# Optimization experiments

Measured on AMD Instinct MI355X. Metric: run time of the kernel, lower is better.

## Reference

```python
import jax, jax.numpy as jnp
import numpy as np

C_IN, D_MODEL, TAO, M = 7, 512, 3, 5
KERNELS = D_MODEL // C_IN              # 73
LEFTOUT = D_MODEL - C_IN * KERNELS     # 1
B, L = 32, 4096


def setup_inputs() -> dict:
    key = jax.random.key(0)
    k1, k2, k3, k4, k5 = jax.random.split(key, 5)
    x = jax.random.normal(k1, (B, L, C_IN), dtype=jnp.float32)
    # kaiming_normal fan_in, leaky_relu (negative_slope=0.01): gain^2/fan_in
    fan_in = (M + 1) * 3
    std = float(np.sqrt(2.0 / (fan_in * (1.0 + 0.01 ** 2))))
    conv_w = jax.random.normal(k2, (KERNELS, M + 1, 3), dtype=jnp.float32) * std
    bound = float(1.0 / np.sqrt(fan_in))
    conv_b = jax.random.uniform(k3, (KERNELS,), jnp.float32, -bound, bound)
    leftout_w = jax.random.uniform(k4, (LEFTOUT, M + 1, 3), jnp.float32, -bound, bound)
    leftout_b = jax.random.uniform(k5, (LEFTOUT,), jnp.float32, -bound, bound)
    return {"x": x, "conv_w": conv_w, "conv_b": conv_b,
            "leftout_w": leftout_w, "leftout_b": leftout_b}


def _circ_conv1d(inp, w, b):
    # inp: [N, Cin, L]; w: [Cout, Cin, 3]; circular padding of 1 on each side
    xp = jnp.concatenate([inp[..., -1:], inp, inp[..., :1]], axis=-1)
    y = jax.lax.conv_general_dilated(xp, w, window_strides=(1,), padding='VALID',
                                     dimension_numbers=('NCH', 'OIH', 'NCH'))
    return y + b[None, :, None]


def reference(x, conv_w, conv_b, leftout_w, leftout_b):
    b, n, c = x.shape  # [B, L, C_IN]
    # delay-coordinate embedding: emb[b, t, c, i] = x[b, t - i*tao, c], zero for t < m*tao
    idx = jnp.arange(n)[:, None] - jnp.arange(M + 1)[None, :] * TAO   # [L, m+1]
    g = x[:, jnp.clip(idx, 0, n - 1), :]                              # [B, L, m+1, C]
    valid = (jnp.arange(n) >= M * TAO)[None, :, None, None]
    g = jnp.where(valid, g, jnp.zeros((), x.dtype))
    # chunk j (over channels) is [B, m+1, L]; all share the same conv -> batch over B*C
    chunks = jnp.transpose(g, (0, 3, 2, 1))                           # [B, C, m+1, L]
    flat = chunks.reshape(b * c, M + 1, n)
    y = _circ_conv1d(flat, conv_w, conv_b).reshape(b, c * KERNELS, n)  # [B, C*K, L]
    y_left = _circ_conv1d(chunks[:, -1], leftout_w, leftout_b)         # [B, LEFTOUT, L]
    out = jnp.concatenate([y, y_left], axis=1)                         # [B, D_MODEL, L]
    return jnp.transpose(out, (0, 2, 1))                               # [B, L, D_MODEL]
```

## Files before the change

kernel.cpp:

```cpp
#include <hip/hip_runtime.h>

#define C_IN     7
#define D_MODEL  512
#define TAO      3
#define M_TAPS   5
#define KERNELS  73
#define B_SZ     32
#define L_SZ     4096
#define TB       64
#define NTB      (L_SZ / TB)
#define ROWS     (TB + 17)
#define SHIFT    3
#define RPAD     88
#define CHUNK    8
#define NCH      (TB / CHUNK)

__global__ __launch_bounds__(512, 6) void trc_conv_kernel(
    const float* __restrict__ x,
    const float* __restrict__ conv_w,
    const float* __restrict__ conv_b,
    const float* __restrict__ leftout_w,
    const float* __restrict__ leftout_b,
    float* __restrict__ out)
{
    __shared__ float xs[C_IN][RPAD];
    __shared__ __align__(16) float buf[8][2][CHUNK][64];

    const int tid = threadIdx.x;
    const int wv  = tid >> 6;
    const int ln  = tid & 63;
    const int b   = blockIdx.x / NTB;
    const int tb  = blockIdx.x % NTB;
    const int t0  = tb * TB;

    const float* xb = x + (size_t)b * L_SZ * C_IN;
    for (int i = tid; i < ROWS * C_IN; i += 512) {
        int r = i / C_IN, c = i - r * C_IN;
        int g = t0 - 16 + r;
        if (g < 0)      g += L_SZ;
        if (g >= L_SZ)  g -= L_SZ;
        xs[c][r + SHIFT] = xb[(size_t)g * C_IN + c];
    }
    __syncthreads();

    const int d = tid;
    int ch;
    const float* wsrc;
    float bias;
    if (d < C_IN * KERNELS) {
        ch = d / KERNELS;
        int o = d - ch * KERNELS;
        wsrc = conv_w + o * 18;
        bias = conv_b[o];
    } else {
        ch = C_IN - 1;
        wsrc = leftout_w;
        bias = leftout_b[0];
    }
    const float* __restrict__ rowp = &xs[ch][SHIFT];

    float wreg[18];
    #pragma unroll
    for (int j = 0; j < 18; ++j) {
        int k = j % 3;
        int m = (15 + k - j) / 3;
        wreg[j] = wsrc[m * 3 + k];
    }

    const bool first = (tb == 0), last = (tb == NTB - 1);

    auto edge_eval = [&](int tl) -> float {
        float acc = bias;
        #pragma unroll
        for (int k = 0; k < 3; ++k) {
            int tt = t0 + tl + k - 1;
            if (tt < 0)      tt += L_SZ;
            if (tt >= L_SZ)  tt -= L_SZ;
            if (tt >= M_TAPS * TAO) {
                int lt = tl + 15 + k;
                #pragma unroll
                for (int m = 0; m < 6; ++m)
                    acc = fmaf(rowp[lt - 3 * m], wreg[15 + k - 3 * m], acc);
            }
        }
        return acc;
    };

    float* __restrict__ bufw = &buf[wv][0][0][0];
    const int lr = ln >> 4, lc = ln & 15;
    float4* base4 = (float4*)(out + ((size_t)b * L_SZ + t0) * D_MODEL + wv * 64);

    float win[25];
    #pragma unroll
    for (int q = 0; q < 17; ++q) win[q] = rowp[q];

    float4 r0, r1;

    for (int c = 0; c < NCH; ++c) {
        float* __restrict__ bc = bufw + (c & 1) * (CHUNK * 64);

        {
            float4 f0 = *(const float4*)&rowp[8 * c + 17];
            float4 f1 = *(const float4*)&rowp[8 * c + 21];
            win[17] = f0.x; win[18] = f0.y; win[19] = f0.z; win[20] = f0.w;
            win[21] = f1.x; win[22] = f1.y; win[23] = f1.z; win[24] = f1.w;
        }

        #pragma unroll
        for (int i = 0; i < CHUNK; ++i) {
            float acc = bias;
            #pragma unroll
            for (int j = 0; j < 18; ++j)
                acc = fmaf(win[i + j], wreg[j], acc);
            bc[i * 64 + ln] = acc;
        }
        #pragma unroll
        for (int q = 0; q < 17; ++q) win[q] = win[q + 8];

        if (first && c < 2) {
            for (int i = 0; i < CHUNK; ++i)
                bc[i * 64 + ln] = edge_eval(c * CHUNK + i);
        }
        if (last && c == NCH - 1) {
            bc[(CHUNK - 1) * 64 + ln] = edge_eval(TB - 1);
        }

        const float4* bv = (const float4*)bc;
        float4 n0 = bv[ln];
        float4 n1 = bv[ln + 64];
        __builtin_amdgcn_sched_barrier(0);

        if (c > 0) {
            base4[(size_t)((c - 1) * CHUNK + 0 + lr) * (D_MODEL / 4) + lc] = r0;
            base4[(size_t)((c - 1) * CHUNK + 4 + lr) * (D_MODEL / 4) + lc] = r1;
        }
        r0 = n0; r1 = n1;
    }
    base4[(size_t)((NCH - 1) * CHUNK + 0 + lr) * (D_MODEL / 4) + lc] = r0;
    base4[(size_t)((NCH - 1) * CHUNK + 4 + lr) * (D_MODEL / 4) + lc] = r1;
}

extern "C" void kernel_launch(void* const* d_in, const int* in_sizes, int n_in,
                              void* d_out, int out_size, void* d_ws, size_t ws_size,
                              hipStream_t stream) {
    const float* x          = (const float*)d_in[0];
    const float* conv_w     = (const float*)d_in[1];
    const float* conv_b     = (const float*)d_in[2];
    const float* leftout_w  = (const float*)d_in[3];
    const float* leftout_b  = (const float*)d_in[4];
    float* out = (float*)d_out;

    dim3 grid(B_SZ * NTB);
    trc_conv_kernel<<<grid, 512, 0, stream>>>(x, conv_w, conv_b,
                                              leftout_w, leftout_b, out);
}
```

Baseline: 49.69 us.

## Add dedicated store wavefront with block-wide double-buffered LDS staging

Adds a ninth wavefront that acts as a producer-consumer store engine. The 8 compute waves write each 8-row chunk into a shared block-wide double buffer, and the store wave writes full 2 KB output rows to global memory. Compute and store waves synchronize with a block barrier per chunk. This is meant to decouple global stores from the FMA work and give fully contiguous row writes. In exchange it adds a barrier every chunk, and the occupancy hint drops from 6 to 4 blocks, with one wave that does little arithmetic.

```diff
diff --git a/kernel.cpp b/kernel.cpp
--- a/kernel.cpp
+++ b/kernel.cpp
@@ -14,8 +14,18 @@
 #define RPAD     88
 #define CHUNK    8
 #define NCH      (TB / CHUNK)
+#define NT       576
 
-__global__ __launch_bounds__(512, 6) void trc_conv_kernel(
+#define LDS_BARRIER()                                          \
+    do {                                                       \
+        __builtin_amdgcn_sched_barrier(0);                     \
+        asm volatile("s_waitcnt lgkmcnt(0)" ::: "memory");     \
+        __builtin_amdgcn_sched_barrier(0);                     \
+        __builtin_amdgcn_s_barrier();                          \
+        __builtin_amdgcn_sched_barrier(0);                     \
+    } while (0)
+
+__global__ __launch_bounds__(NT, 4) void trc_conv_kernel(
     const float* __restrict__ x,
     const float* __restrict__ conv_w,
     const float* __restrict__ conv_b,
@@ -24,7 +34,7 @@
     float* __restrict__ out)
 {
     __shared__ float xs[C_IN][RPAD];
-    __shared__ __align__(16) float buf[8][2][CHUNK][64];
+    __shared__ __align__(16) float buf[2][CHUNK][D_MODEL];
 
     const int tid = threadIdx.x;
     const int wv  = tid >> 6;
@@ -34,8 +44,8 @@
     const int t0  = tb * TB;
 
     const float* xb = x + (size_t)b * L_SZ * C_IN;
-    for (int i = tid; i < ROWS * C_IN; i += 512) {
-        int r = i / C_IN, c = i - r * C_IN;
+    if (tid < ROWS * C_IN) {
+        int r = tid / C_IN, c = tid - r * C_IN;
         int g = t0 - 16 + r;
         if (g < 0)      g += L_SZ;
         if (g >= L_SZ)  g -= L_SZ;
@@ -43,101 +53,120 @@
     }
     __syncthreads();
 
-    const int d = tid;
-    int ch;
-    const float* wsrc;
-    float bias;
-    if (d < C_IN * KERNELS) {
-        ch = d / KERNELS;
-        int o = d - ch * KERNELS;
-        wsrc = conv_w + o * 18;
-        bias = conv_b[o];
-    } else {
-        ch = C_IN - 1;
-        wsrc = leftout_w;
-        bias = leftout_b[0];
-    }
-    const float* __restrict__ rowp = &xs[ch][SHIFT];
+    if (wv < 8) {
+        const int d = tid;
+        int ch;
+        const float* wsrc;
+        float bias;
+        if (d < C_IN * KERNELS) {
+            ch = d / KERNELS;
+            int o = d - ch * KERNELS;
+            wsrc = conv_w + o * 18;
+            bias = conv_b[o];
+        } else {
+            ch = C_IN - 1;
+            wsrc = leftout_w;
+            bias = leftout_b[0];
+        }
+        const float* __restrict__ rowp = &xs[ch][SHIFT];
 
-    float wreg[18];
-    #pragma unroll
-    for (int j = 0; j < 18; ++j) {
-        int k = j % 3;
-        int m = (15 + k - j) / 3;
-        wreg[j] = wsrc[m * 3 + k];
-    }
-
-    const bool first = (tb == 0), last = (tb == NTB - 1);
-
-    auto edge_eval = [&](int tl) -> float {
-        float acc = bias;
+        float wreg[18];
         #pragma unroll
-        for (int k = 0; k < 3; ++k) {
-            int tt = t0 + tl + k - 1;
-            if (tt < 0)      tt += L_SZ;
-            if (tt >= L_SZ)  tt -= L_SZ;
-            if (tt >= M_TAPS * TAO) {
-                int lt = tl + 15 + k;
-                #pragma unroll
-                for (int m = 0; m < 6; ++m)
-                    acc = fmaf(rowp[lt - 3 * m], wreg[15 + k - 3 * m], acc);
-            }
-        }
-        return acc;
-    };
-
-    float* __restrict__ bufw = &buf[wv][0][0][0];
-    const int lr = ln >> 4, lc = ln & 15;
-    float4* base4 = (float4*)(out + ((size_t)b * L_SZ + t0) * D_MODEL + wv * 64);
-
-    float win[25];
-    #pragma unroll
-    for (int q = 0; q < 17; ++q) win[q] = rowp[q];
-
-    float4 r0, r1;
-
-    for (int c = 0; c < NCH; ++c) {
-        float* __restrict__ bc = bufw + (c & 1) * (CHUNK * 64);
-
-        {
-            float4 f0 = *(const float4*)&rowp[8 * c + 17];
-            float4 f1 = *(const float4*)&rowp[8 * c + 21];
-            win[17] = f0.x; win[18] = f0.y; win[19] = f0.z; win[20] = f0.w;
-            win[21] = f1.x; win[22] = f1.y; win[23] = f1.z; win[24] = f1.w;
+        for (int j = 0; j < 18; ++j) {
+            int k = j % 3;
+            int m = (15 + k - j) / 3;
+            wreg[j] = wsrc[m * 3 + k];
         }
 
-        #pragma unroll
-        for (int i = 0; i < CHUNK; ++i) {
+        const bool first = (tb == 0), last = (tb == NTB - 1);
+
+        auto edge_eval = [&](int tl) -> float {
             float acc = bias;
             #pragma unroll
-            for (int j = 0; j < 18; ++j)
-                acc = fmaf(win[i + j], wreg[j], acc);
-            bc[i * 64 + ln] = acc;
+            for (int k = 0; k < 3; ++k) {
+                int tt = t0 + tl + k - 1;
+                if (tt < 0)      tt += L_SZ;
+                if (tt >= L_SZ)  tt -= L_SZ;
+                if (tt >= M_TAPS * TAO) {
+                    int lt = tl + 15 + k;
+                    #pragma unroll
+                    for (int m = 0; m < 6; ++m)
+                        acc = fmaf(rowp[lt - 3 * m], wreg[15 + k - 3 * m], acc);
+                }
+            }
+            return acc;
+        };
+
+        float win[25];
+        #pragma unroll
+        for (int q = 0; q < 17; ++q) win[q] = rowp[q];
+
+        for (int c = 0; c < NCH; ++c) {
+            float* __restrict__ bc = &buf[c & 1][0][0];
+
+            {
+                float4 f0 = *(const float4*)&rowp[8 * c + 17];
+                float4 f1 = *(const float4*)&rowp[8 * c + 21];
+                win[17] = f0.x; win[18] = f0.y; win[19] = f0.z; win[20] = f0.w;
+                win[21] = f1.x; win[22] = f1.y; win[23] = f1.z; win[24] = f1.w;
+            }
+
+            #pragma unroll
+            for (int i = 0; i < CHUNK; ++i) {
+                float acc = bias;
+                #pragma unroll
+                for (int j = 0; j < 18; ++j)
+                    acc = fmaf(win[i + j], wreg[j], acc);
+                bc[i * D_MODEL + d] = acc;
+            }
+            #pragma unroll
+            for (int q = 0; q < 17; ++q) win[q] = win[q + 8];
+
+            if (first && c < 2) {
+                for (int i = 0; i < CHUNK; ++i)
+                    bc[i * D_MODEL + d] = edge_eval(c * CHUNK + i);
+            }
+            if (last && c == NCH - 1) {
+                bc[(CHUNK - 1) * D_MODEL + d] = edge_eval(TB - 1);
+            }
+
+            LDS_BARRIER();
         }
-        #pragma unroll
-        for (int q = 0; q < 17; ++q) win[q] = win[q + 8];
+    } else {
+        float4* o4 = (float4*)(out + ((size_t)b * L_SZ + t0) * D_MODEL);
 
-        if (first && c < 2) {
-            for (int i = 0; i < CHUNK; ++i)
-                bc[i * 64 + ln] = edge_eval(c * CHUNK + i);
+        for (int c = 0; c < NCH; ++c) {
+            if (c > 0) {
+                const float4* bv = (const float4*)&buf[(c - 1) & 1][0][0];
+                float4 v[8];
+                #pragma unroll
+                for (int g = 0; g < 8; ++g) v[g] = bv[g * 64 + ln];
+                #pragma unroll
+                for (int g = 0; g < 8; ++g)
+                    o4[(size_t)(c - 1) * 1024 + g * 64 + ln] = v[g];
+                #pragma unroll
+                for (int g = 0; g < 8; ++g) v[g] = bv[(g + 8) * 64 + ln];
+                #pragma unroll
+                for (int g = 0; g < 8; ++g)
+                    o4[(size_t)(c - 1) * 1024 + (g + 8) * 64 + ln] = v[g];
+            }
+            LDS_BARRIER();
         }
-        if (last && c == NCH - 1) {
-            bc[(CHUNK - 1) * 64 + ln] = edge_eval(TB - 1);
+        {
+            const float4* bv = (const float4*)&buf[(NCH - 1) & 1][0][0];
+            float4 v[8];
+            #pragma unroll
+            for (int g = 0; g < 8; ++g) v[g] = bv[g * 64 + ln];
+            #pragma unroll
+            for (int g = 0; g < 8; ++g)
+                o4[(size_t)(NCH - 1) * 1024 + g * 64 + ln] = v[g];
+            #pragma unroll
+            for (int g = 0; g < 8; ++g) v[g] = bv[(g + 8) * 64 + ln];
+            #pragma unroll
+            for (int g = 0; g < 8; ++g)
+                o4[(size_t)(NCH - 1) * 1024 + (g + 8) * 64 + ln] = v[g];
         }
-
-        const float4* bv = (const float4*)bc;
-        float4 n0 = bv[ln];
-        float4 n1 = bv[ln + 64];
-        __builtin_amdgcn_sched_barrier(0);
-
-        if (c > 0) {
-            base4[(size_t)((c - 1) * CHUNK + 0 + lr) * (D_MODEL / 4) + lc] = r0;
-            base4[(size_t)((c - 1) * CHUNK + 4 + lr) * (D_MODEL / 4) + lc] = r1;
-        }
-        r0 = n0; r1 = n1;
     }
-    base4[(size_t)((NCH - 1) * CHUNK + 0 + lr) * (D_MODEL / 4) + lc] = r0;
-    base4[(size_t)((NCH - 1) * CHUNK + 4 + lr) * (D_MODEL / 4) + lc] = r1;
 }
 
 extern "C" void kernel_launch(void* const* d_in, const int* in_sizes, int n_in,
@@ -151,6 +180,6 @@
     float* out = (float*)d_out;
 
     dim3 grid(B_SZ * NTB);
-    trc_conv_kernel<<<grid, 512, 0, stream>>>(x, conv_w, conv_b,
-                                              leftout_w, leftout_b, out);
+    trc_conv_kernel<<<grid, NT, 0, stream>>>(x, conv_w, conv_b,
+                                             leftout_w, leftout_b, out);
 }
```

Result: slower. 54.59 us (+9.9%).
